# Kernel tuning notes

Hardware: AMD Instinct MI355X
Metric: run time of the kernel (lower is better)

The kernel has to match this reference:

```python
import jax, jax.numpy as jnp
import numpy as np

B, T, L, DC, DW, H, V = 128, 256, 4, 128, 128, 256, 6000
NEG = -1e30

def _lstm(x, c, h, kernel, bias):
    # TF BasicLSTMCell, forget_bias=0, gate order i, j, f, o
    z = jnp.concatenate([x, h], axis=-1) @ kernel + bias
    i, j, f, o = jnp.split(z, 4, axis=-1)
    nc = c * jax.nn.sigmoid(f) + jax.nn.sigmoid(i) * jnp.tanh(j)
    nh = jnp.tanh(nc) * jax.nn.sigmoid(o)
    return nc, nh

def _forward(chars, char_emb, reset_W, reset_b, com_W, com_b, lstm_kernel, lstm_bias, pred_W, pred_b, score_U, bos):
    Bn, Tn = chars.shape
    dt = char_emb.dtype
    # init agenda entry: BoS vector through LSTM from zero state
    c0 = jnp.zeros((Bn, H), dt)
    h0 = jnp.zeros((Bn, H), dt)
    x0 = jnp.broadcast_to(bos, (Bn, DW))
    c1, h1 = _lstm(x0, c0, h0, lstm_kernel, lstm_bias)
    pred0 = jnp.tanh(h1 @ pred_W + pred_b)
    # rolling buffer over the last L agenda entries (slot w-1 = position t-w)
    buf_pred = jnp.repeat(pred0[:, None, :], L, axis=1)
    buf_c = jnp.repeat(c1[:, None, :], L, axis=1)
    buf_h = jnp.repeat(h1[:, None, :], L, axis=1)
    # windows[t, b, j] = char at position t-j (age j), front-padded
    padded = jnp.pad(chars, ((0, 0), (L - 1, 0)))
    gi = jnp.arange(Tn)[:, None] + (L - 1) - jnp.arange(L)[None, :]
    windows = jnp.transpose(padded[:, gi], (1, 0, 2))  # [T, B, L]
    wlens = jnp.arange(1, L + 1)
    cmask = (jnp.arange(L)[None, :] < wlens[:, None]).astype(dt)  # [W, C]
    inv_len = (1.0 / wlens).astype(dt)

    def step(carry, xs):
        buf_pred, buf_c, buf_h = carry
        window, t = xs
        emb = char_emb[window]  # [B, L, DC] (ages 0..L-1)
        # per-wlen reset gate (separate weights per word length)
        g = jax.nn.sigmoid(jnp.einsum('bcd,wde->bwce', emb, reset_W) + reset_b[None, :, None, :])
        proj = jnp.tanh(jnp.einsum('bwcd,de->bwce', g * emb[:, None], com_W) + com_b)  # [B,W,C,DW]
        word = jnp.einsum('bwce,wc->bwe', proj, cmask) * inv_len[None, :, None]  # [B,W,DW] mean over the wlen chars
        score = jnp.sum((buf_pred + score_U) * word, axis=-1)  # [B,W] local score vs prev prediction
        score = jnp.where((wlens <= t + 1)[None, :], score, NEG)
        best = jnp.argmax(score, axis=1)  # greedy choice of word length
        b3 = best[:, None, None]
        word_b = jnp.take_along_axis(word, b3, axis=1)[:, 0]
        c_prev = jnp.take_along_axis(buf_c, b3, axis=1)[:, 0]
        h_prev = jnp.take_along_axis(buf_h, b3, axis=1)[:, 0]
        nc, nh = _lstm(word_b, c_prev, h_prev, lstm_kernel, lstm_bias)
        npred = jnp.tanh(nh @ pred_W + pred_b)
        carry = (jnp.concatenate([npred[:, None], buf_pred[:, :-1]], axis=1),
                 jnp.concatenate([nc[:, None], buf_c[:, :-1]], axis=1),
                 jnp.concatenate([nh[:, None], buf_h[:, :-1]], axis=1))
        best_score = jnp.take_along_axis(score, best[:, None], axis=1)[:, 0]
        return carry, (best_score, best + 1)

    _, (scores, wl) = jax.lax.scan(step, (buf_pred, buf_c, buf_h), (windows, jnp.arange(Tn)))
    return scores.T, wl.T  # [B,T] best local score, [B,T] chosen word length

def setup_inputs() -> dict:
    key = jax.random.key(0)
    ks = jax.random.split(key, 12)
    f = lambda k, s: 0.1 * jax.random.normal(k, s, dtype=jnp.float32)
    return {
        'chars': jax.random.randint(ks[0], (B, T), 0, V, dtype=jnp.int32),
        'char_emb': f(ks[1], (V, DC)),
        'reset_W': f(ks[2], (L, DC, DC)),
        'reset_b': f(ks[3], (L, DC)),
        'com_W': f(ks[4], (DC, DW)),
        'com_b': f(ks[5], (DW,)),
        'lstm_kernel': f(ks[6], (DW + H, 4 * H)),
        'lstm_bias': jnp.zeros((4 * H,), jnp.float32),
        'pred_W': f(ks[7], (H, DW)),
        'pred_b': f(ks[8], (DW,)),
        'score_U': f(ks[9], (DW,)),
        'bos': f(ks[10], (DW,)),
    }

def reference(chars, char_emb, reset_W, reset_b, com_W, com_b, lstm_kernel, lstm_bias, pred_W, pred_b, score_U, bos):
    return _forward(chars, char_emb, reset_W, reset_b, com_W, com_b, lstm_kernel, lstm_bias, pred_W, pred_b, score_U, bos)
```

## Files before the change

### kernel.cpp

```cpp
#include <hip/hip_runtime.h>

#define B_ 128
#define T_ 256
#define L_ 4
#define DC_ 128
#define DW_ 128
#define H_ 256
#define V_ 6000
#define Z4_ 1024
#define S_ 4
#define R_ 2
#define G_ 64
#define NEGF -1e30f

#define WS_VTAB  4096
#define WS_NH    (WS_VTAB + V_*L_*DW_*4)
#define WS_PP    (WS_NH + (size_t)2*G_*R_*H_*8)

typedef unsigned long long u64w;

__device__ __forceinline__ float sigm(float x) { return 1.0f / (1.0f + expf(-x)); }
__device__ __forceinline__ void pub64(u64w* p, float v, unsigned stamp) {
  u64w w = ((u64w)__float_as_uint(v) << 32) | (u64w)stamp;
  __hip_atomic_store(p, w, __ATOMIC_RELAXED, __HIP_MEMORY_SCOPE_AGENT);
}
__device__ __forceinline__ u64w ld64(const u64w* p) {
  return __hip_atomic_load(p, __ATOMIC_RELAXED, __HIP_MEMORY_SCOPE_AGENT);
}
__device__ __forceinline__ float hi32(u64w w) {
  return __uint_as_float((unsigned)(w >> 32));
}
__device__ __forceinline__ float bcast(float v, int l) {
  return __int_as_float(__builtin_amdgcn_readlane(__float_as_int(v), l));
}
__device__ __forceinline__ int amax4(const float* sc) {
  float bs = sc[0]; int bw = 0;
  if (sc[1] > bs) { bs = sc[1]; bw = 1; }
  if (sc[2] > bs) { bs = sc[2]; bw = 2; }
  if (sc[3] > bs) { bs = sc[3]; bw = 3; }
  return bw;
}
__device__ __forceinline__ float invlen(int w) {
  return (w == 0) ? 1.0f : (w == 1) ? 0.5f : (w == 2) ? (1.0f / 3.0f) : 0.25f;
}

__global__ __launch_bounds__(512) void vtab_kernel(
    const float* __restrict__ char_emb, const float* __restrict__ reset_W,
    const float* __restrict__ reset_b, const float* __restrict__ com_W,
    const float* __restrict__ com_b, float* __restrict__ Vtab)
{
  const int v = blockIdx.x;
  const int tid = threadIdx.x;
  const int w = tid >> 7;
  const int e = tid & 127;
  __shared__ float emb[DC_];
  __shared__ float ge[L_][DC_];
  if (tid < DC_) emb[tid] = char_emb[v * DC_ + tid];
  __syncthreads();
  float acc = reset_b[w * DC_ + e];
  const float* W = reset_W + (size_t)w * DC_ * DC_;
  #pragma unroll 8
  for (int k = 0; k < DC_; ++k) acc = fmaf(emb[k], W[k * DC_ + e], acc);
  ge[w][e] = sigm(acc) * emb[e];
  __syncthreads();
  float acc2 = com_b[e];
  #pragma unroll 8
  for (int k = 0; k < DC_; ++k) acc2 = fmaf(ge[w][k], com_W[k * DW_ + e], acc2);
  Vtab[((size_t)v * L_ + w) * DW_ + e] = tanhf(acc2);
}

__global__ __launch_bounds__(512, 2) void seq_kernel(
    const int* __restrict__ chars, const float* __restrict__ Vtab,
    const float* __restrict__ Kmat, const float* __restrict__ lstm_bias,
    const float* __restrict__ pred_W, const float* __restrict__ pred_b,
    const float* __restrict__ score_U, const float* __restrict__ bos,
    float* __restrict__ out, u64w* __restrict__ nh_mb, u64w* __restrict__ pp_mb)
{
  const int blk = blockIdx.x;
  const int s = blk >> 6;
  const int g = blk & 63;
  const int tid = threadIdx.x;
  const int lane = tid & 63;
  const int wv = tid >> 6;
  const int c = tid & 255;
  const int koff = (tid < 256) ? 0 : 192;
  const int colg = (c >> 6) * H_ + s * 64 + (c & 63);
  const int row0 = g * R_;

  float wreg[192];
  #pragma unroll
  for (int i = 0; i < 192; ++i)
    wreg[i] = Kmat[(size_t)(koff + i) * Z4_ + colg];

  __shared__ float ringVt[R_][4][512];
  __shared__ float pring[4][R_][DW_];
  __shared__ float zring[4][R_][256];
  __shared__ float cring[4][R_][64];
  __shared__ float zhA[R_][256];
  __shared__ float zhB[R_][256];
  __shared__ float zxL[R_][256];
  __shared__ float predWL[64][128];
  __shared__ float h1tmp[H_];
  __shared__ int   charsL[R_][T_];
  __shared__ float biasC[256], UL[128], pbL[128];
  __shared__ float scL[R_][L_];

  if (tid < 256) biasC[tid] = lstm_bias[(tid >> 6) * H_ + s * 64 + (tid & 63)];
  if (tid < 128) { UL[tid] = score_U[tid]; pbL[tid] = pred_b[tid]; }
  for (int i = tid; i < 64 * 128; i += 512)
    predWL[i >> 7][i & 127] = pred_W[(size_t)(s * 64 + (i >> 7)) * DW_ + (i & 127)];
  for (int i = tid; i < R_ * T_; i += 512)
    charsL[i >> 8][i & 255] = chars[(row0 + (i >> 8)) * T_ + (i & 255)];
  for (int i = tid; i < R_ * 4 * 512; i += 512) ((float*)ringVt)[i] = 0.0f;
  __syncthreads();

  {
    float* zb = &zring[0][0][0];
    for (int c2 = tid; c2 < Z4_; c2 += 512) {
      float a = lstm_bias[c2];
      #pragma unroll 8
      for (int k = 0; k < DC_; ++k) a = fmaf(bos[k], Kmat[(size_t)k * Z4_ + c2], a);
      zb[c2] = a;
    }
    __syncthreads();
    if (tid < H_) {
      float zi = zb[tid], zj = zb[H_ + tid], zo = zb[3 * H_ + tid];
      float nc = sigm(zi) * tanhf(zj);
      float nh = tanhf(nc) * sigm(zo);
      h1tmp[tid] = nh;
      int hl = tid - s * 64;
      if (hl >= 0 && hl < 64) {
        #pragma unroll
        for (int q = 0; q < 4; ++q)
          #pragma unroll
          for (int r = 0; r < R_; ++r) cring[q][r][hl] = nc;
      }
    }
    __syncthreads();
    {
      int kq = tid >> 7, e = tid & 127;
      float a = 0.0f;
      #pragma unroll 8
      for (int k = kq * 64; k < kq * 64 + 64; ++k)
        a = fmaf(h1tmp[k], pred_W[(size_t)k * DW_ + e], a);
      ((float*)zhA)[kq * 128 + e] = a;
    }
    __syncthreads();
    if (tid < 128) {
      const float* pa = (const float*)zhA;
      float p = tanhf(pbL[tid] + pa[tid] + pa[128 + tid] + pa[256 + tid] + pa[384 + tid]);
      #pragma unroll
      for (int q = 0; q < 4; ++q)
        #pragma unroll
        for (int r = 0; r < R_; ++r) pring[q][r][tid] = p;
    }
    __syncthreads();
    {
      float a = 0.0f;
      if (tid < 256) {
        #pragma unroll
        for (int k = 0; k < 64; ++k) a = fmaf(h1tmp[k], wreg[128 + k], a);
      } else {
        #pragma unroll
        for (int k = 0; k < 192; ++k) a = fmaf(h1tmp[64 + k], wreg[k], a);
      }
      __syncthreads();
      if (tid < 256) zhA[0][c] = a; else zhB[0][c] = a;
    }
    __syncthreads();
    if (tid < 256) {
      float z1 = zhA[0][tid] + zhB[0][tid];
      #pragma unroll
      for (int q = 0; q < 4; ++q)
        #pragma unroll
        for (int r = 0; r < R_; ++r) zring[q][r][tid] = z1;
    }
    __syncthreads();
  }

  for (int t = 0; t < T_; ++t) {
    const int slot = t & 3;
    const int parR = (t - 1) & 1;
    const int parW = t & 1;
    const unsigned stR = (unsigned)t;
    const unsigned stW = (unsigned)(t + 1);

    if ((wv >> 1) == 1) {
      int i2 = tid & 127;
      #pragma unroll
      for (int r = 0; r < R_; ++r) {
        const float* vp = Vtab + (size_t)charsL[r][t] * 512;
        #pragma unroll
        for (int q = 0; q < 4; ++q) ringVt[r][slot][q * 128 + i2] = vp[q * 128 + i2];
      }
    }

    if (t > 0) {
      const u64w* nb = nh_mb + ((size_t)parR * G_ + g) * (R_ * H_);
      if (wv < 2) {
        u64w nw0, nw1;
        for (;;) {
          nw0 = ld64(nb + lane);
          nw1 = ld64(nb + H_ + lane);
          int ok = ((unsigned)nw0 == stR) & ((unsigned)nw1 == stR);
          if (__all(ok)) break;
          __builtin_amdgcn_s_sleep(1);
        }
        float nv0 = hi32(nw0), nv1 = hi32(nw1);
        float z0 = 0.0f, z1 = 0.0f;
        #pragma unroll
        for (int k = 0; k < 64; ++k) {
          float w = wreg[128 + k];
          z0 = fmaf(bcast(nv0, k), w, z0);
          z1 = fmaf(bcast(nv1, k), w, z1);
        }
        zhA[0][c] = z0; zhA[1][c] = z1;
        const u64w* ppb = pp_mb + ((size_t)parR * G_ + g) * (S_ * R_ * 128) + wv * 128;
        u64w pw0[S_], pw1[S_];
        for (;;) {
          #pragma unroll
          for (int sp = 0; sp < S_; ++sp) {
            pw0[sp] = ld64(ppb + (size_t)sp * (R_ * 128) + lane);
            pw1[sp] = ld64(ppb + (size_t)sp * (R_ * 128) + lane + 64);
          }
          int ok = 1;
          #pragma unroll
          for (int sp = 0; sp < S_; ++sp)
            ok &= ((unsigned)pw0[sp] == stR) & ((unsigned)pw1[sp] == stR);
          if (__all(ok)) break;
          __builtin_amdgcn_s_sleep(1);
        }
        float a0 = pbL[lane], a1 = pbL[lane + 64];
        #pragma unroll
        for (int sp = 0; sp < S_; ++sp) {
          a0 += hi32(pw0[sp]);
          a1 += hi32(pw1[sp]);
        }
        int ps = (t - 1) & 3;
        pring[ps][wv][lane] = tanhf(a0);
        pring[ps][wv][lane + 64] = tanhf(a1);
      } else if (wv < 4) {
        u64w nw0, nw1;
        for (;;) {
          nw0 = ld64(nb + lane);
          nw1 = ld64(nb + H_ + lane);
          int ok = ((unsigned)nw0 == stR) & ((unsigned)nw1 == stR);
          if (__all(ok)) break;
          __builtin_amdgcn_s_sleep(1);
        }
        float nv0 = hi32(nw0), nv1 = hi32(nw1);
        float z0 = 0.0f, z1 = 0.0f;
        #pragma unroll
        for (int k = 0; k < 64; ++k) {
          float w = wreg[128 + k];
          z0 = fmaf(bcast(nv0, k), w, z0);
          z1 = fmaf(bcast(nv1, k), w, z1);
        }
        zhA[0][c] = z0; zhA[1][c] = z1;
      } else {
        u64w nw[2][3];
        for (;;) {
          #pragma unroll
          for (int r = 0; r < 2; ++r)
            #pragma unroll
            for (int j = 0; j < 3; ++j)
              nw[r][j] = ld64(nb + (size_t)r * H_ + 64 + j * 64 + lane);
          int ok = 1;
          #pragma unroll
          for (int r = 0; r < 2; ++r)
            #pragma unroll
            for (int j = 0; j < 3; ++j)
              ok &= ((unsigned)nw[r][j] == stR);
          if (__all(ok)) break;
          __builtin_amdgcn_s_sleep(1);
        }
        float a0 = 0.0f, a1 = 0.0f;
        #pragma unroll
        for (int j = 0; j < 3; ++j) {
          float nv0 = hi32(nw[0][j]), nv1 = hi32(nw[1][j]);
          #pragma unroll
          for (int k = 0; k < 64; ++k) {
            float w = wreg[j * 64 + k];
            a0 = fmaf(bcast(nv0, k), w, a0);
            a1 = fmaf(bcast(nv1, k), w, a1);
          }
        }
        zhB[0][c] = a0; zhB[1][c] = a1;
      }
    }
    __syncthreads();

    if (t > 0) {
      int r = tid >> 8, cc = tid & 255;
      zring[(t - 1) & 3][r][cc] = zhA[r][cc] + zhB[r][cc];
    }
    {
      int r = wv >> 2, w = wv & 3;
      int ps = (t - 1 - w) & 3;
      float il = invlen(w);
      float acc = 0.0f;
      #pragma unroll
      for (int hf = 0; hf < 2; ++hf) {
        int e = lane + hf * 64;
        float sa = 0.0f;
        #pragma unroll
        for (int c2 = 0; c2 < L_; ++c2)
          if (c2 <= w) sa += ringVt[r][(t - c2) & 3][w * 128 + e];
        acc = fmaf(pring[ps][r][e] + UL[e], sa * il, acc);
      }
      #pragma unroll
      for (int off = 32; off; off >>= 1) acc += __shfl_down(acc, off);
      if (lane == 0) scL[r][w] = (w <= t) ? acc : NEGF;
    }
    __syncthreads();

    if (tid < 256) {
      float vt0[2], vt1[2];
      #pragma unroll
      for (int r = 0; r < 2; ++r) {
        int bw = amax4(scL[r]);
        float il = invlen(bw);
        float v0 = 0.f, v1 = 0.f;
        #pragma unroll
        for (int c2 = 0; c2 < L_; ++c2)
          if (c2 <= bw) {
            v0 += ringVt[r][(t - c2) & 3][bw * 128 + lane];
            v1 += ringVt[r][(t - c2) & 3][bw * 128 + 64 + lane];
          }
        vt0[r] = v0 * il; vt1[r] = v1 * il;
      }
      float a0 = 0.f, a1 = 0.f;
      #pragma unroll
      for (int k = 0; k < 64; ++k) {
        float w0 = wreg[k], w1 = wreg[64 + k];
        a0 = fmaf(bcast(vt0[0], k), w0, a0);
        a1 = fmaf(bcast(vt0[1], k), w0, a1);
        a0 = fmaf(bcast(vt1[0], k), w1, a0);
        a1 = fmaf(bcast(vt1[1], k), w1, a1);
      }
      zxL[0][c] = a0; zxL[1][c] = a1;
      if (s == 0 && tid < R_) {
        int bw = amax4(scL[tid]);
        out[(row0 + tid) * T_ + t] = scL[tid][bw];
        out[B_ * T_ + (row0 + tid) * T_ + t] = (float)(bw + 1);
      }
    }
    __syncthreads();

    if (tid < 128) {
      int r = wv, hl = lane;
      int bw = amax4(scL[r]);
      int zs = (t - 1 - bw) & 3;
      float zg[4];
      #pragma unroll
      for (int gi = 0; gi < 4; ++gi) {
        int cc = gi * 64 + hl;
        zg[gi] = biasC[cc] + zring[zs][r][cc] + zxL[r][cc];
      }
      float cp = cring[zs][r][hl];
      float nc = cp * sigm(zg[2]) + sigm(zg[0]) * tanhf(zg[1]);
      float nh = tanhf(nc) * sigm(zg[3]);
      pub64(&nh_mb[((size_t)parW * G_ + g) * (R_ * H_) + (size_t)r * H_ + s * 64 + hl],
            nh, stW);
      cring[slot][r][hl] = nc;
      float p0 = 0.f, p1 = 0.f;
      #pragma unroll
      for (int kk = 0; kk < 64; ++kk) {
        float nb2 = __shfl(nh, kk, 64);
        p0 = fmaf(nb2, predWL[kk][lane], p0);
        p1 = fmaf(nb2, predWL[kk][lane + 64], p1);
      }
      u64w* pb = pp_mb + ((size_t)parW * G_ + g) * (S_ * R_ * 128)
               + (size_t)s * (R_ * 128) + (size_t)r * 128;
      pub64(pb + lane, p0, stW);
      pub64(pb + lane + 64, p1, stW);
    }
  }
}

extern "C" void kernel_launch(void* const* d_in, const int* in_sizes, int n_in,
                              void* d_out, int out_size, void* d_ws, size_t ws_size,
                              hipStream_t stream) {
  const int*   chars     = (const int*)d_in[0];
  const float* char_emb  = (const float*)d_in[1];
  const float* reset_W   = (const float*)d_in[2];
  const float* reset_b   = (const float*)d_in[3];
  const float* com_W     = (const float*)d_in[4];
  const float* com_b     = (const float*)d_in[5];
  const float* lstm_k    = (const float*)d_in[6];
  const float* lstm_bias = (const float*)d_in[7];
  const float* pred_W    = (const float*)d_in[8];
  const float* pred_b    = (const float*)d_in[9];
  const float* score_U   = (const float*)d_in[10];
  const float* bos       = (const float*)d_in[11];

  char* ws = (char*)d_ws;
  float* Vtab = (float*)(ws + WS_VTAB);
  u64w* nh_mb = (u64w*)(ws + WS_NH);
  u64w* pp_mb = (u64w*)(ws + WS_PP);

  vtab_kernel<<<V_, 512, 0, stream>>>(char_emb, reset_W, reset_b, com_W, com_b, Vtab);
  seq_kernel<<<256, 512, 0, stream>>>(chars, Vtab, lstm_k, lstm_bias, pred_W,
                                      pred_b, score_U, bos, (float*)d_out,
                                      nh_mb, pp_mb);
}
```

Before: 2.211 ms.

## Use XCC-local L2 polling and plain stores when a block group shares one XCC

Each block records its XCC id from the hardware register, and the blocks of a row group check whether they all sit on the same XCC. If they do, the mailbox spin loops poll with sc0 loads that are served from the shared L2, falling back to the original agent-scope load every sixteenth try, and the publish side uses plain stores instead of agent-scope atomic stores. This targets the latency of the cross-block handoffs on every timestep. It relies on XCC-local L2 coherence, which holds only when the whole group lands on one XCC; otherwise the original path runs. A stale XCC magic stamp left in the workspace from an earlier launch could also mislead the check.

```diff
diff --git a/kernel.cpp b/kernel.cpp
--- a/kernel.cpp
+++ b/kernel.cpp
@@ -16,16 +16,34 @@
 #define WS_VTAB  4096
 #define WS_NH    (WS_VTAB + V_*L_*DW_*4)
 #define WS_PP    (WS_NH + (size_t)2*G_*R_*H_*8)
+#define WS_XCC   (WS_PP + (size_t)2*G_*S_*R_*128*8)
+
+#define XCC_MAGIC 0xC0FFEE01u
 
 typedef unsigned long long u64w;
 
 __device__ __forceinline__ float sigm(float x) { return 1.0f / (1.0f + expf(-x)); }
+__device__ __forceinline__ u64w packw(float v, unsigned stamp) {
+  return ((u64w)__float_as_uint(v) << 32) | (u64w)stamp;
+}
 __device__ __forceinline__ void pub64(u64w* p, float v, unsigned stamp) {
-  u64w w = ((u64w)__float_as_uint(v) << 32) | (u64w)stamp;
+  __hip_atomic_store(p, packw(v, stamp), __ATOMIC_RELAXED, __HIP_MEMORY_SCOPE_AGENT);
+}
+__device__ __forceinline__ void pub64u(u64w* p, unsigned v, unsigned stamp) {
+  u64w w = ((u64w)v << 32) | (u64w)stamp;
   __hip_atomic_store(p, w, __ATOMIC_RELAXED, __HIP_MEMORY_SCOPE_AGENT);
 }
 __device__ __forceinline__ u64w ld64(const u64w* p) {
   return __hip_atomic_load(p, __ATOMIC_RELAXED, __HIP_MEMORY_SCOPE_AGENT);
+}
+__device__ __forceinline__ u64w ld64_l2_issue(const u64w* p) {
+  u64w r;
+  asm volatile("global_load_dwordx2 %0, %1, off sc0" : "=&v"(r) : "v"(p));
+  return r;
+}
+__device__ __forceinline__ void vm_wait0() {
+  asm volatile("s_waitcnt vmcnt(0)" ::: "memory");
+  __builtin_amdgcn_sched_barrier(0);
 }
 __device__ __forceinline__ float hi32(u64w w) {
   return __uint_as_float((unsigned)(w >> 32));
@@ -74,7 +92,8 @@
     const float* __restrict__ Kmat, const float* __restrict__ lstm_bias,
     const float* __restrict__ pred_W, const float* __restrict__ pred_b,
     const float* __restrict__ score_U, const float* __restrict__ bos,
-    float* __restrict__ out, u64w* __restrict__ nh_mb, u64w* __restrict__ pp_mb)
+    float* __restrict__ out, u64w* __restrict__ nh_mb, u64w* __restrict__ pp_mb,
+    u64w* __restrict__ xcc_mb)
 {
   const int blk = blockIdx.x;
   const int s = blk >> 6;
@@ -86,6 +105,11 @@
   const int koff = (tid < 256) ? 0 : 192;
   const int colg = (c >> 6) * H_ + s * 64 + (c & 63);
   const int row0 = g * R_;
+
+  if (tid == 0) {
+    unsigned xcc = __builtin_amdgcn_s_getreg(20 | (31 << 11)) & 0xFFu;
+    pub64u(&xcc_mb[(size_t)s * G_ + g], xcc, XCC_MAGIC);
+  }
 
   float wreg[192];
   #pragma unroll
@@ -104,6 +128,7 @@
   __shared__ int   charsL[R_][T_];
   __shared__ float biasC[256], UL[128], pbL[128];
   __shared__ float scL[R_][L_];
+  __shared__ int   fastL2s;
 
   if (tid < 256) biasC[tid] = lstm_bias[(tid >> 6) * H_ + s * 64 + (tid & 63)];
   if (tid < 128) { UL[tid] = score_U[tid]; pbL[tid] = pred_b[tid]; }
@@ -175,8 +200,23 @@
         #pragma unroll
         for (int r = 0; r < R_; ++r) zring[q][r][tid] = z1;
     }
-    __syncthreads();
   }
+
+  if (tid == 0) {
+    unsigned v0 = 0xFFFFu, okf = 1;
+    #pragma unroll
+    for (int sp = 0; sp < S_; ++sp) {
+      u64w w;
+      do { w = ld64(&xcc_mb[(size_t)sp * G_ + g]); } while ((unsigned)w != XCC_MAGIC);
+      unsigned xv = (unsigned)(w >> 32);
+      if (sp == 0) v0 = xv;
+      okf &= (xv == v0);
+    }
+    okf &= (v0 < 8u);
+    fastL2s = (int)okf;
+  }
+  __syncthreads();
+  const bool fastL2 = (fastL2s != 0);
 
   for (int t = 0; t < T_; ++t) {
     const int slot = t & 3;
@@ -199,12 +239,28 @@
       const u64w* nb = nh_mb + ((size_t)parR * G_ + g) * (R_ * H_);
       if (wv < 2) {
         u64w nw0, nw1;
-        for (;;) {
-          nw0 = ld64(nb + lane);
-          nw1 = ld64(nb + H_ + lane);
-          int ok = ((unsigned)nw0 == stR) & ((unsigned)nw1 == stR);
-          if (__all(ok)) break;
-          __builtin_amdgcn_s_sleep(1);
+        if (fastL2) {
+          int rd = 0;
+          for (;;) {
+            if ((rd++ & 15) == 15) {
+              nw0 = ld64(nb + lane); nw1 = ld64(nb + H_ + lane);
+            } else {
+              nw0 = ld64_l2_issue(nb + lane);
+              nw1 = ld64_l2_issue(nb + H_ + lane);
+              vm_wait0();
+            }
+            int ok = ((unsigned)nw0 == stR) & ((unsigned)nw1 == stR);
+            if (__all(ok)) break;
+            __builtin_amdgcn_s_sleep(1);
+          }
+        } else {
+          for (;;) {
+            nw0 = ld64(nb + lane);
+            nw1 = ld64(nb + H_ + lane);
+            int ok = ((unsigned)nw0 == stR) & ((unsigned)nw1 == stR);
+            if (__all(ok)) break;
+            __builtin_amdgcn_s_sleep(1);
+          }
         }
         float nv0 = hi32(nw0), nv1 = hi32(nw1);
         float z0 = 0.0f, z1 = 0.0f;
@@ -217,18 +273,44 @@
         zhA[0][c] = z0; zhA[1][c] = z1;
         const u64w* ppb = pp_mb + ((size_t)parR * G_ + g) * (S_ * R_ * 128) + wv * 128;
         u64w pw0[S_], pw1[S_];
-        for (;;) {
-          #pragma unroll
-          for (int sp = 0; sp < S_; ++sp) {
-            pw0[sp] = ld64(ppb + (size_t)sp * (R_ * 128) + lane);
-            pw1[sp] = ld64(ppb + (size_t)sp * (R_ * 128) + lane + 64);
-          }
-          int ok = 1;
-          #pragma unroll
-          for (int sp = 0; sp < S_; ++sp)
-            ok &= ((unsigned)pw0[sp] == stR) & ((unsigned)pw1[sp] == stR);
-          if (__all(ok)) break;
-          __builtin_amdgcn_s_sleep(1);
+        if (fastL2) {
+          int rd = 0;
+          for (;;) {
+            if ((rd++ & 15) == 15) {
+              #pragma unroll
+              for (int sp = 0; sp < S_; ++sp) {
+                pw0[sp] = ld64(ppb + (size_t)sp * (R_ * 128) + lane);
+                pw1[sp] = ld64(ppb + (size_t)sp * (R_ * 128) + lane + 64);
+              }
+            } else {
+              #pragma unroll
+              for (int sp = 0; sp < S_; ++sp) {
+                pw0[sp] = ld64_l2_issue(ppb + (size_t)sp * (R_ * 128) + lane);
+                pw1[sp] = ld64_l2_issue(ppb + (size_t)sp * (R_ * 128) + lane + 64);
+              }
+              vm_wait0();
+            }
+            int ok = 1;
+            #pragma unroll
+            for (int sp = 0; sp < S_; ++sp)
+              ok &= ((unsigned)pw0[sp] == stR) & ((unsigned)pw1[sp] == stR);
+            if (__all(ok)) break;
+            __builtin_amdgcn_s_sleep(1);
+          }
+        } else {
+          for (;;) {
+            #pragma unroll
+            for (int sp = 0; sp < S_; ++sp) {
+              pw0[sp] = ld64(ppb + (size_t)sp * (R_ * 128) + lane);
+              pw1[sp] = ld64(ppb + (size_t)sp * (R_ * 128) + lane + 64);
+            }
+            int ok = 1;
+            #pragma unroll
+            for (int sp = 0; sp < S_; ++sp)
+              ok &= ((unsigned)pw0[sp] == stR) & ((unsigned)pw1[sp] == stR);
+            if (__all(ok)) break;
+            __builtin_amdgcn_s_sleep(1);
+          }
         }
         float a0 = pbL[lane], a1 = pbL[lane + 64];
         #pragma unroll
@@ -241,12 +323,28 @@
         pring[ps][wv][lane + 64] = tanhf(a1);
       } else if (wv < 4) {
         u64w nw0, nw1;
-        for (;;) {
-          nw0 = ld64(nb + lane);
-          nw1 = ld64(nb + H_ + lane);
-          int ok = ((unsigned)nw0 == stR) & ((unsigned)nw1 == stR);
-          if (__all(ok)) break;
-          __builtin_amdgcn_s_sleep(1);
+        if (fastL2) {
+          int rd = 0;
+          for (;;) {
+            if ((rd++ & 15) == 15) {
+              nw0 = ld64(nb + lane); nw1 = ld64(nb + H_ + lane);
+            } else {
+              nw0 = ld64_l2_issue(nb + lane);
+              nw1 = ld64_l2_issue(nb + H_ + lane);
+              vm_wait0();
+            }
+            int ok = ((unsigned)nw0 == stR) & ((unsigned)nw1 == stR);
+            if (__all(ok)) break;
+            __builtin_amdgcn_s_sleep(1);
+          }
+        } else {
+          for (;;) {
+            nw0 = ld64(nb + lane);
+            nw1 = ld64(nb + H_ + lane);
+            int ok = ((unsigned)nw0 == stR) & ((unsigned)nw1 == stR);
+            if (__all(ok)) break;
+            __builtin_amdgcn_s_sleep(1);
+          }
         }
         float nv0 = hi32(nw0), nv1 = hi32(nw1);
         float z0 = 0.0f, z1 = 0.0f;
@@ -259,20 +357,48 @@
         zhA[0][c] = z0; zhA[1][c] = z1;
       } else {
         u64w nw[2][3];
-        for (;;) {
-          #pragma unroll
-          for (int r = 0; r < 2; ++r)
+        if (fastL2) {
+          int rd = 0;
+          for (;;) {
+            if ((rd++ & 15) == 15) {
+              #pragma unroll
+              for (int r = 0; r < 2; ++r)
+                #pragma unroll
+                for (int j = 0; j < 3; ++j)
+                  nw[r][j] = ld64(nb + (size_t)r * H_ + 64 + j * 64 + lane);
+            } else {
+              #pragma unroll
+              for (int r = 0; r < 2; ++r)
+                #pragma unroll
+                for (int j = 0; j < 3; ++j)
+                  nw[r][j] = ld64_l2_issue(nb + (size_t)r * H_ + 64 + j * 64 + lane);
+              vm_wait0();
+            }
+            int ok = 1;
             #pragma unroll
-            for (int j = 0; j < 3; ++j)
-              nw[r][j] = ld64(nb + (size_t)r * H_ + 64 + j * 64 + lane);
-          int ok = 1;
-          #pragma unroll
-          for (int r = 0; r < 2; ++r)
+            for (int r = 0; r < 2; ++r)
+              #pragma unroll
+              for (int j = 0; j < 3; ++j)
+                ok &= ((unsigned)nw[r][j] == stR);
+            if (__all(ok)) break;
+            __builtin_amdgcn_s_sleep(1);
+          }
+        } else {
+          for (;;) {
             #pragma unroll
-            for (int j = 0; j < 3; ++j)
-              ok &= ((unsigned)nw[r][j] == stR);
-          if (__all(ok)) break;
-          __builtin_amdgcn_s_sleep(1);
+            for (int r = 0; r < 2; ++r)
+              #pragma unroll
+              for (int j = 0; j < 3; ++j)
+                nw[r][j] = ld64(nb + (size_t)r * H_ + 64 + j * 64 + lane);
+            int ok = 1;
+            #pragma unroll
+            for (int r = 0; r < 2; ++r)
+              #pragma unroll
+              for (int j = 0; j < 3; ++j)
+                ok &= ((unsigned)nw[r][j] == stR);
+            if (__all(ok)) break;
+            __builtin_amdgcn_s_sleep(1);
+          }
         }
         float a0 = 0.0f, a1 = 0.0f;
         #pragma unroll
@@ -360,8 +486,9 @@
       float cp = cring[zs][r][hl];
       float nc = cp * sigm(zg[2]) + sigm(zg[0]) * tanhf(zg[1]);
       float nh = tanhf(nc) * sigm(zg[3]);
-      pub64(&nh_mb[((size_t)parW * G_ + g) * (R_ * H_) + (size_t)r * H_ + s * 64 + hl],
-            nh, stW);
+      u64w* pnh = &nh_mb[((size_t)parW * G_ + g) * (R_ * H_) + (size_t)r * H_ + s * 64 + hl];
+      if (fastL2) *pnh = packw(nh, stW);
+      else        __hip_atomic_store(pnh, packw(nh, stW), __ATOMIC_RELAXED, __HIP_MEMORY_SCOPE_AGENT);
       cring[slot][r][hl] = nc;
       float p0 = 0.f, p1 = 0.f;
       #pragma unroll
@@ -372,8 +499,13 @@
       }
       u64w* pb = pp_mb + ((size_t)parW * G_ + g) * (S_ * R_ * 128)
                + (size_t)s * (R_ * 128) + (size_t)r * 128;
-      pub64(pb + lane, p0, stW);
-      pub64(pb + lane + 64, p1, stW);
+      if (fastL2) {
+        pb[lane] = packw(p0, stW);
+        pb[lane + 64] = packw(p1, stW);
+      } else {
+        pub64(pb + lane, p0, stW);
+        pub64(pb + lane + 64, p1, stW);
+      }
     }
   }
 }
@@ -398,9 +530,10 @@
   float* Vtab = (float*)(ws + WS_VTAB);
   u64w* nh_mb = (u64w*)(ws + WS_NH);
   u64w* pp_mb = (u64w*)(ws + WS_PP);
+  u64w* xcc_mb = (u64w*)(ws + WS_XCC);
 
   vtab_kernel<<<V_, 512, 0, stream>>>(char_emb, reset_W, reset_b, com_W, com_b, Vtab);
   seq_kernel<<<256, 512, 0, stream>>>(chars, Vtab, lstm_k, lstm_bias, pred_W,
                                       pred_b, score_U, bos, (float*)d_out,
-                                      nh_mb, pp_mb);
-}
+                                      nh_mb, pp_mb, xcc_mb);
+}
```

Measured after the change: 2.901 ms. 31.2% more time.

## Spread recurrent h-matmul across idle phases and prioritize LSTM cell waves

Applied to the files above, without the earlier changes.

Previously waves 4-7 each spun on the neighbour h values and then did the full 192-deep h-part matmul before the first barrier, which sat on the per-step critical path. Now only wave 4 waits for the h values and stages them in shared memory. Waves 4-7 then do two thirds of the matmul while waves 0-3 compute the scores, with each of those waves now handling both rows. The last third overlaps with the zx computation, and zring is written at that point. The LSTM cell and publish section also gets raised wave priority. The cost is an extra LDS staging buffer and a heavier score workload per wave.

```diff
diff --git a/kernel.cpp b/kernel.cpp
--- a/kernel.cpp
+++ b/kernel.cpp
@@ -99,6 +99,7 @@
   __shared__ float zhA[R_][256];
   __shared__ float zhB[R_][256];
   __shared__ float zxL[R_][256];
+  __shared__ float nhL[6][64];
   __shared__ float predWL[64][128];
   __shared__ float h1tmp[H_];
   __shared__ int   charsL[R_][T_];
@@ -257,7 +258,7 @@
           z1 = fmaf(bcast(nv1, k), w, z1);
         }
         zhA[0][c] = z0; zhA[1][c] = z1;
-      } else {
+      } else if (wv == 4) {
         u64w nw[2][3];
         for (;;) {
           #pragma unroll
@@ -274,43 +275,52 @@
           if (__all(ok)) break;
           __builtin_amdgcn_s_sleep(1);
         }
-        float a0 = 0.0f, a1 = 0.0f;
-        #pragma unroll
-        for (int j = 0; j < 3; ++j) {
-          float nv0 = hi32(nw[0][j]), nv1 = hi32(nw[1][j]);
-          #pragma unroll
-          for (int k = 0; k < 64; ++k) {
-            float w = wreg[j * 64 + k];
-            a0 = fmaf(bcast(nv0, k), w, a0);
-            a1 = fmaf(bcast(nv1, k), w, a1);
-          }
-        }
-        zhB[0][c] = a0; zhB[1][c] = a1;
-      }
-    }
-    __syncthreads();
-
-    if (t > 0) {
-      int r = tid >> 8, cc = tid & 255;
-      zring[(t - 1) & 3][r][cc] = zhA[r][cc] + zhB[r][cc];
-    }
-    {
-      int r = wv >> 2, w = wv & 3;
-      int ps = (t - 1 - w) & 3;
-      float il = invlen(w);
-      float acc = 0.0f;
-      #pragma unroll
-      for (int hf = 0; hf < 2; ++hf) {
-        int e = lane + hf * 64;
-        float sa = 0.0f;
-        #pragma unroll
-        for (int c2 = 0; c2 < L_; ++c2)
-          if (c2 <= w) sa += ringVt[r][(t - c2) & 3][w * 128 + e];
-        acc = fmaf(pring[ps][r][e] + UL[e], sa * il, acc);
-      }
-      #pragma unroll
-      for (int off = 32; off; off >>= 1) acc += __shfl_down(acc, off);
-      if (lane == 0) scL[r][w] = (w <= t) ? acc : NEGF;
+        #pragma unroll
+        for (int r = 0; r < 2; ++r)
+          #pragma unroll
+          for (int j = 0; j < 3; ++j)
+            nhL[r * 3 + j][lane] = hi32(nw[r][j]);
+      }
+    }
+    __syncthreads();
+
+    if (wv < 4) {
+      #pragma unroll
+      for (int r = 0; r < 2; ++r) {
+        int w = wv;
+        int ps = (t - 1 - w) & 3;
+        float il = invlen(w);
+        float acc = 0.0f;
+        #pragma unroll
+        for (int hf = 0; hf < 2; ++hf) {
+          int e = lane + hf * 64;
+          float sa = 0.0f;
+          #pragma unroll
+          for (int c2 = 0; c2 < L_; ++c2)
+            if (c2 <= w) sa += ringVt[r][(t - c2) & 3][w * 128 + e];
+          acc = fmaf(pring[ps][r][e] + UL[e], sa * il, acc);
+        }
+        #pragma unroll
+        for (int off = 32; off; off >>= 1) acc += __shfl_down(acc, off);
+        if (lane == 0) scL[r][w] = (w <= t) ? acc : NEGF;
+      }
+    } else if (t > 0) {
+      float nv00 = nhL[0][lane], nv10 = nhL[3][lane];
+      float nv01 = nhL[1][lane], nv11 = nhL[4][lane];
+      float z0 = 0.0f, z1 = 0.0f;
+      #pragma unroll
+      for (int k = 0; k < 64; ++k) {
+        float w = wreg[k];
+        z0 = fmaf(bcast(nv00, k), w, z0);
+        z1 = fmaf(bcast(nv10, k), w, z1);
+      }
+      #pragma unroll
+      for (int k = 0; k < 64; ++k) {
+        float w = wreg[64 + k];
+        z0 = fmaf(bcast(nv01, k), w, z0);
+        z1 = fmaf(bcast(nv11, k), w, z1);
+      }
+      zhB[0][c] = z0; zhB[1][c] = z1;
     }
     __syncthreads();
 
@@ -344,10 +354,23 @@
         out[(row0 + tid) * T_ + t] = scL[tid][bw];
         out[B_ * T_ + (row0 + tid) * T_ + t] = (float)(bw + 1);
       }
+    } else if (t > 0) {
+      float nv02 = nhL[2][lane], nv12 = nhL[5][lane];
+      float z0 = zhB[0][c], z1 = zhB[1][c];
+      #pragma unroll
+      for (int k = 0; k < 64; ++k) {
+        float w = wreg[128 + k];
+        z0 = fmaf(bcast(nv02, k), w, z0);
+        z1 = fmaf(bcast(nv12, k), w, z1);
+      }
+      int zs2 = (t - 1) & 3;
+      zring[zs2][0][c] = zhA[0][c] + z0;
+      zring[zs2][1][c] = zhA[1][c] + z1;
     }
     __syncthreads();
 
     if (tid < 128) {
+      __builtin_amdgcn_s_setprio(1);
       int r = wv, hl = lane;
       int bw = amax4(scL[r]);
       int zs = (t - 1 - bw) & 3;
@@ -374,6 +397,7 @@
                + (size_t)s * (R_ * 128) + (size_t)r * 128;
       pub64(pb + lane, p0, stW);
       pub64(pb + lane + 64, p1, stW);
+      __builtin_amdgcn_s_setprio(0);
     }
   }
 }
```

After: 2.450 ms. 1.11x slower.
